# Optimization experiments

Measured on AMD Instinct MI355X. Metric: run time of the kernel, lower is better.

Reference implementation:

```python
import jax, jax.numpy as jnp
import numpy as np

EPS = 0.1
N_ITERS = 20


def setup_inputs() -> dict:
    key = jax.random.key(0)
    B, N = 8, 2048
    D = jax.random.normal(key, (B, N, N), dtype=jnp.float32)
    mask = jnp.ones((B, N), dtype=bool)
    return {"D": D, "mask": mask}


def reference(D, mask):
    # pad_2d[b,i,j] = True if row i or col j is padding
    pad_col = ~mask[:, None, :]          # [B,1,N]
    pad_row = ~mask[:, :, None]          # [B,N,1]
    pad_2d = pad_col | pad_row           # [B,N,N]
    log_K = jnp.where(pad_2d, -jnp.inf, -D / EPS)

    def body(lk, _):
        lk = lk - jax.nn.logsumexp(lk, axis=2, keepdims=True)  # row normalize
        lk = lk - jax.nn.logsumexp(lk, axis=1, keepdims=True)  # col normalize
        return lk, None

    log_K, _ = jax.lax.scan(body, log_K, None, length=N_ITERS)
    P = jnp.exp(log_K)
    n_real = jnp.maximum(mask.sum(axis=1).astype(D.dtype), 1.0)  # clamp(min=1)
    per_sample = (P * D).sum(axis=(1, 2)) / n_real
    return per_sample.mean()
```

## Files before the change

kernel.cpp:

```cpp
#include <hip/hip_runtime.h>


#ifndef __has_builtin
#define __has_builtin(x) 0
#endif

__device__ __forceinline__ float ex2(float x) {
#if __has_builtin(__builtin_amdgcn_exp2f)
  return __builtin_amdgcn_exp2f(x);
#else
  return exp2f(x);
#endif
}
__device__ __forceinline__ float lg2(float x) {
#if __has_builtin(__builtin_amdgcn_logf)
  return __builtin_amdgcn_logf(x);
#else
  return __log2f(x);
#endif
}

constexpr int   Bc    = 8;
constexpr int   Nc    = 2048;
constexpr int   NBLK  = 256;
constexpr int   NTHR  = 512;
constexpr int   WPB   = 8;
constexpr int   RPW   = 8;
constexpr int   RPB   = 64;
constexpr int   SL    = 32;
constexpr int   NIT   = 20;
constexpr int   FB    = 64;
constexpr float K2    = -14.426950408889634f;
constexpr float SCALE = -4.2306346e-06f;

__device__ __forceinline__ float f16lo(unsigned u) {
  return (float)__builtin_bit_cast(_Float16, (unsigned short)(u & 0xffffu));
}
__device__ __forceinline__ float f16hi(unsigned u) {
  return (float)__builtin_bit_cast(_Float16, (unsigned short)(u >> 16));
}
__device__ __forceinline__ unsigned packh(float x, float y) {
  unsigned short hx = __builtin_bit_cast(unsigned short, (_Float16)x);
  unsigned short hy = __builtin_bit_cast(unsigned short, (_Float16)y);
  return (unsigned)hx | ((unsigned)hy << 16);
}

typedef float fx4 __attribute__((ext_vector_type(4)));

__device__ __forceinline__ void st_sc(float* p, float4 v) {
  fx4 vv;
  vv.x = v.x; vv.y = v.y; vv.z = v.z; vv.w = v.w;
  asm volatile("global_store_dwordx4 %0, %1, off sc0 sc1"
               :
               : "v"(p), "v"(vv)
               : "memory");
}
__device__ __forceinline__ void st_sc1(float* p, float v) {
  asm volatile("global_store_dword %0, %1, off sc0 sc1"
               :
               : "v"(p), "v"(v)
               : "memory");
}

__device__ __forceinline__ void arrive(unsigned* f, unsigned epv) {
  asm volatile("s_waitcnt vmcnt(0)" ::: "memory");
  __syncthreads();
  if (threadIdx.x == 0)
    __hip_atomic_store(f, epv, __ATOMIC_RELAXED, __HIP_MEMORY_SCOPE_AGENT);
}
__device__ __forceinline__ void waitfor(const unsigned* fb_, unsigned epv) {
  const int t = threadIdx.x;
  if (t < 64) {
    bool ok = (t >= SL);
    for (;;) {
      if (t < SL)
        ok = __hip_atomic_load(&fb_[t], __ATOMIC_RELAXED,
                               __HIP_MEMORY_SCOPE_AGENT) >= epv;
      if (__ballot(ok) == ~0ull) break;
      __builtin_amdgcn_s_sleep(2);
    }
  }
  __syncthreads();
}

__global__ void k_init(unsigned* flags, float* out) {
  __hip_atomic_store(&flags[threadIdx.x], 0u, __ATOMIC_RELAXED,
                     __HIP_MEMORY_SCOPE_AGENT);
  if (threadIdx.x == 0)
    __hip_atomic_store(out, 0.f, __ATOMIC_RELAXED, __HIP_MEMORY_SCOPE_AGENT);
}

__global__ __launch_bounds__(NTHR, 2) void sink(const float* __restrict__ D,
                                                _Float16* __restrict__ A,
                                                float* __restrict__ Sp,
                                                float* __restrict__ Tp,
                                                float* __restrict__ cg,
                                                unsigned* __restrict__ f1,
                                                unsigned* __restrict__ f2,
                                                float* __restrict__ out) {
  __shared__ float colpart[WPB * Nc];
  __shared__ float cl[Nc];
  __shared__ float rl[RPB];

  const int t    = threadIdx.x;
  const int lane = t & 63;
  const int w    = t >> 6;
  const int blk  = blockIdx.x;
  const int b    = blk >> 5;
  const int s    = blk & 31;
  const long long row0 = (long long)b * Nc + (long long)s * RPB;
  unsigned* f1b = f1 + b * FB;
  unsigned* f2b = f2 + b * FB;

  if (t == 0) __builtin_amdgcn_fence(__ATOMIC_ACQUIRE, "agent");
  __syncthreads();

  for (int r = 0; r < RPW; ++r) {
    long long grow = row0 + (w * RPW + r);
    const float* dp = D + grow * Nc + lane * 8;
    _Float16*    ap = A + grow * Nc + lane * 8;
    #pragma unroll
    for (int c = 0; c < 4; ++c) {
      float4 x0 = *(const float4*)(dp + c * 512);
      float4 x1 = *(const float4*)(dp + c * 512 + 4);
      uint4 h;
      h.x = packh(K2 * x0.x, K2 * x0.y);
      h.y = packh(K2 * x0.z, K2 * x0.w);
      h.z = packh(K2 * x1.x, K2 * x1.y);
      h.w = packh(K2 * x1.z, K2 * x1.w);
      *(uint4*)(ap + c * 512) = h;
    }
  }
  for (int j = t; j < Nc; j += NTHR) cl[j] = 0.f;
  if (t < RPB) rl[t] = 0.f;
  __syncthreads();

  const _Float16* abase = A + (row0 + (long long)w * RPW) * Nc + lane * 8;

  #pragma unroll 1
  for (int it = 0; it < NIT; ++it) {
    const unsigned epv = (unsigned)(it + 1);
    const bool lastIt = (it == NIT - 1);
    float* SpIt = Sp + (size_t)it * (NBLK * Nc);
    float* cgIt = cg + (size_t)it * (Bc * Nc);

    float cs[32];
    #pragma unroll
    for (int c = 0; c < 4; ++c) {
      float4 q0 = *(const float4*)&cl[c * 512 + lane * 8];
      float4 q1 = *(const float4*)&cl[c * 512 + lane * 8 + 4];
      cs[c * 8 + 0] = q0.x; cs[c * 8 + 1] = q0.y; cs[c * 8 + 2] = q0.z; cs[c * 8 + 3] = q0.w;
      cs[c * 8 + 4] = q1.x; cs[c * 8 + 5] = q1.y; cs[c * 8 + 6] = q1.z; cs[c * 8 + 7] = q1.w;
    }
    float colacc[32], colaccT[32];
    #pragma unroll
    for (int k = 0; k < 32; ++k) { colacc[k] = 0.f; colaccT[k] = 0.f; }

    auto process = [&](const uint4 (&bf)[4], int lrow) {
      float shift = rl[lrow];
      const unsigned uu[16] = {bf[0].x, bf[0].y, bf[0].z, bf[0].w,
                               bf[1].x, bf[1].y, bf[1].z, bf[1].w,
                               bf[2].x, bf[2].y, bf[2].z, bf[2].w,
                               bf[3].x, bf[3].y, bf[3].z, bf[3].w};
      float e[32];
      float rs = 0.f;
      #pragma unroll
      for (int q = 0; q < 16; ++q) {
        float e0 = ex2(f16lo(uu[q]) - cs[2 * q] - shift);
        float e1 = ex2(f16hi(uu[q]) - cs[2 * q + 1] - shift);
        e[2 * q] = e0; e[2 * q + 1] = e1;
        rs += e0 + e1;
      }
      #pragma unroll
      for (int off = 1; off < 64; off <<= 1) rs += __shfl_xor(rs, off, 64);
      float inv = 1.0f / rs;
      #pragma unroll
      for (int k = 0; k < 32; ++k) colacc[k] += e[k] * inv;
      if (lastIt) {
        #pragma unroll
        for (int q = 0; q < 16; ++q) {
          colaccT[2 * q]     += e[2 * q] * inv * f16lo(uu[q]);
          colaccT[2 * q + 1] += e[2 * q + 1] * inv * f16hi(uu[q]);
        }
      }
      if (lane == 0) rl[lrow] = shift + lg2(rs);
    };

    uint4 cA[4], cB[4];
    #pragma unroll
    for (int c = 0; c < 4; ++c) cA[c] = *(const uint4*)(abase + c * 512);
    #pragma unroll
    for (int c = 0; c < 4; ++c) cB[c] = *(const uint4*)(abase + Nc + c * 512);
    #pragma unroll 1
    for (int rp = 0; rp < RPW / 2; ++rp) {
      uint4 nA[4], nB[4];
      #pragma unroll
      for (int c = 0; c < 4; ++c) { nA[c] = cA[c]; nB[c] = cB[c]; }
      if (rp < RPW / 2 - 1) {
        const _Float16* ap = abase + (size_t)(2 * rp + 2) * Nc;
        #pragma unroll
        for (int c = 0; c < 4; ++c) nA[c] = *(const uint4*)(ap + c * 512);
        #pragma unroll
        for (int c = 0; c < 4; ++c) nB[c] = *(const uint4*)(ap + Nc + c * 512);
      }
      process(cA, w * RPW + 2 * rp);
      process(cB, w * RPW + 2 * rp + 1);
      #pragma unroll
      for (int c = 0; c < 4; ++c) { cA[c] = nA[c]; cB[c] = nB[c]; }
    }

    #pragma unroll
    for (int c = 0; c < 4; ++c) {
      *(float4*)&colpart[w * Nc + c * 512 + lane * 8] =
          make_float4(colacc[c * 8 + 0], colacc[c * 8 + 1], colacc[c * 8 + 2], colacc[c * 8 + 3]);
      *(float4*)&colpart[w * Nc + c * 512 + lane * 8 + 4] =
          make_float4(colacc[c * 8 + 4], colacc[c * 8 + 5], colacc[c * 8 + 6], colacc[c * 8 + 7]);
    }
    __syncthreads();
    {
      int j0 = t * 4;
      float4 v = *(const float4*)&colpart[j0];
      #pragma unroll
      for (int g = 1; g < WPB; ++g) {
        float4 u = *(const float4*)&colpart[g * Nc + j0];
        v.x += u.x; v.y += u.y; v.z += u.z; v.w += u.w;
      }
      st_sc(SpIt + (size_t)blk * Nc + j0, v);
    }
    if (lastIt) {
      __syncthreads();
      #pragma unroll
      for (int c = 0; c < 4; ++c) {
        *(float4*)&colpart[w * Nc + c * 512 + lane * 8] =
            make_float4(colaccT[c * 8 + 0], colaccT[c * 8 + 1], colaccT[c * 8 + 2], colaccT[c * 8 + 3]);
        *(float4*)&colpart[w * Nc + c * 512 + lane * 8 + 4] =
            make_float4(colaccT[c * 8 + 4], colaccT[c * 8 + 5], colaccT[c * 8 + 6], colaccT[c * 8 + 7]);
      }
      __syncthreads();
      int j0 = t * 4;
      float4 v = *(const float4*)&colpart[j0];
      #pragma unroll
      for (int g = 1; g < WPB; ++g) {
        float4 u = *(const float4*)&colpart[g * Nc + j0];
        v.x += u.x; v.y += u.y; v.z += u.z; v.w += u.w;
      }
      st_sc(Tp + (size_t)blk * Nc + j0, v);
    }

    arrive(&f1b[s], epv);
    waitfor(f1b, epv);

    if (!lastIt) {
      {
        int colL = t & 63, slg = t >> 6;
        const float* bb = SpIt + (size_t)(b * SL) * Nc + s * 64 + colL;
        float v = 0.f;
        #pragma unroll
        for (int k = 0; k < 4; ++k) v += bb[(slg + 8 * k) * Nc];
        colpart[slg * 64 + colL] = v;
      }
      __syncthreads();
      if (t < 64) {
        float S = 0.f;
        #pragma unroll
        for (int g = 0; g < 8; ++g) S += colpart[g * 64 + t];
        st_sc1(cgIt + (size_t)b * Nc + s * 64 + t, cl[s * 64 + t] + lg2(S));
      }
      arrive(&f2b[s], epv);
      waitfor(f2b, epv);
      {
        int j0 = t * 4;
        float4 v = *(const float4*)(cgIt + (size_t)b * Nc + j0);
        *(float4*)&cl[j0] = v;
      }
      __syncthreads();
    } else {
      {
        int colL = t & 63, slg = t >> 6;
        const float* bbS = SpIt + (size_t)(b * SL) * Nc + s * 64 + colL;
        const float* bbT = Tp + (size_t)(b * SL) * Nc + s * 64 + colL;
        float vS = 0.f, vT = 0.f;
        #pragma unroll
        for (int k = 0; k < 4; ++k) {
          vS += bbS[(slg + 8 * k) * Nc];
          vT += bbT[(slg + 8 * k) * Nc];
        }
        colpart[slg * 64 + colL] = vS;
        colpart[512 + slg * 64 + colL] = vT;
      }
      __syncthreads();
      float q = 0.f;
      if (t < 64) {
        float S = 0.f, T = 0.f;
        #pragma unroll
        for (int g = 0; g < 8; ++g) {
          S += colpart[g * 64 + t];
          T += colpart[512 + g * 64 + t];
        }
        q = T / S;
        #pragma unroll
        for (int off = 32; off > 0; off >>= 1) q += __shfl_down(q, off, 64);
        if (t == 0) atomicAdd(out, q * SCALE);
      }
    }
  }
}

extern "C" void kernel_launch(void* const* d_in, const int* in_sizes, int n_in,
                              void* d_out, int out_size, void* d_ws, size_t ws_size,
                              hipStream_t stream) {
  const float* D = (const float*)d_in[0];
  char* p = (char*)d_ws;
  _Float16* A  = (_Float16*)p;  p += (size_t)Bc * Nc * Nc * 2;
  float*    Sp = (float*)p;     p += (size_t)NIT * NBLK * Nc * 4;
  float*    Tp = (float*)p;     p += (size_t)NBLK * Nc * 4;
  float*    cg = (float*)p;     p += (size_t)NIT * Bc * Nc * 4;
  unsigned* flags = (unsigned*)p;
  unsigned* f1 = flags;
  unsigned* f2 = flags + Bc * FB;

  k_init<<<1, 1024, 0, stream>>>(flags, (float*)d_out);
  sink<<<NBLK, NTHR, 0, stream>>>(D, A, Sp, Tp, cg, f1, f2, (float*)d_out);
}
```

Before: 580.1 us.

## Double block count to 512 with 32 rows each and reuse single-iteration scratch

Halves rows per block (32 instead of 64) and launches 512 persistent blocks, 64 slices per batch, so each CU holds two resident blocks and all CUs get work. Cross-block column reductions now span 64 slices with 32 columns each. Scratch buffers Sp and cg are no longer indexed per iteration; they are reused, with atomic relaxed loads so stale cached values are not read. This cuts the workspace footprint, but reuse relies on the flag barriers ordering writes of the next iteration after reads of the previous one, and there are twice as many blocks to synchronise.

```diff
diff --git a/kernel.cpp b/kernel.cpp
--- a/kernel.cpp
+++ b/kernel.cpp
@@ -22,12 +22,12 @@
 
 constexpr int   Bc    = 8;
 constexpr int   Nc    = 2048;
-constexpr int   NBLK  = 256;
+constexpr int   NBLK  = 512;
 constexpr int   NTHR  = 512;
 constexpr int   WPB   = 8;
-constexpr int   RPW   = 8;
-constexpr int   RPB   = 64;
-constexpr int   SL    = 32;
+constexpr int   RPW   = 4;
+constexpr int   RPB   = 32;
+constexpr int   SL    = 64;
 constexpr int   NIT   = 20;
 constexpr int   FB    = 64;
 constexpr float K2    = -14.426950408889634f;
@@ -60,6 +60,9 @@
                :
                : "v"(p), "v"(v)
                : "memory");
+}
+__device__ __forceinline__ float ald(const float* p) {
+  return __hip_atomic_load(p, __ATOMIC_RELAXED, __HIP_MEMORY_SCOPE_AGENT);
 }
 
 __device__ __forceinline__ void arrive(unsigned* f, unsigned epv) {
@@ -106,8 +109,8 @@
   const int lane = t & 63;
   const int w    = t >> 6;
   const int blk  = blockIdx.x;
-  const int b    = blk >> 5;
-  const int s    = blk & 31;
+  const int b    = blk >> 6;
+  const int s    = blk & 63;
   const long long row0 = (long long)b * Nc + (long long)s * RPB;
   unsigned* f1b = f1 + b * FB;
   unsigned* f2b = f2 + b * FB;
@@ -141,8 +144,6 @@
   for (int it = 0; it < NIT; ++it) {
     const unsigned epv = (unsigned)(it + 1);
     const bool lastIt = (it == NIT - 1);
-    float* SpIt = Sp + (size_t)it * (NBLK * Nc);
-    float* cgIt = cg + (size_t)it * (Bc * Nc);
 
     float cs[32];
     #pragma unroll
@@ -225,7 +226,7 @@
         float4 u = *(const float4*)&colpart[g * Nc + j0];
         v.x += u.x; v.y += u.y; v.z += u.z; v.w += u.w;
       }
-      st_sc(SpIt + (size_t)blk * Nc + j0, v);
+      st_sc(Sp + (size_t)blk * Nc + j0, v);
     }
     if (lastIt) {
       __syncthreads();
@@ -252,52 +253,53 @@
 
     if (!lastIt) {
       {
-        int colL = t & 63, slg = t >> 6;
-        const float* bb = SpIt + (size_t)(b * SL) * Nc + s * 64 + colL;
+        int colL = t & 31, slg = t >> 5;
+        const float* bb = Sp + (size_t)(b * SL) * Nc + s * 32 + colL;
         float v = 0.f;
         #pragma unroll
-        for (int k = 0; k < 4; ++k) v += bb[(slg + 8 * k) * Nc];
-        colpart[slg * 64 + colL] = v;
-      }
-      __syncthreads();
-      if (t < 64) {
+        for (int k = 0; k < 4; ++k) v += ald(&bb[(size_t)(slg + 16 * k) * Nc]);
+        colpart[slg * 32 + colL] = v;
+      }
+      __syncthreads();
+      if (t < 32) {
         float S = 0.f;
         #pragma unroll
-        for (int g = 0; g < 8; ++g) S += colpart[g * 64 + t];
-        st_sc1(cgIt + (size_t)b * Nc + s * 64 + t, cl[s * 64 + t] + lg2(S));
+        for (int g = 0; g < 16; ++g) S += colpart[g * 32 + t];
+        st_sc1(cg + (size_t)b * Nc + s * 32 + t, cl[s * 32 + t] + lg2(S));
       }
       arrive(&f2b[s], epv);
       waitfor(f2b, epv);
       {
-        int j0 = t * 4;
-        float4 v = *(const float4*)(cgIt + (size_t)b * Nc + j0);
-        *(float4*)&cl[j0] = v;
+        const float* cgb = cg + (size_t)b * Nc;
+        for (int j = t; j < Nc; j += NTHR) cl[j] = ald(cgb + j);
       }
       __syncthreads();
     } else {
       {
-        int colL = t & 63, slg = t >> 6;
-        const float* bbS = SpIt + (size_t)(b * SL) * Nc + s * 64 + colL;
-        const float* bbT = Tp + (size_t)(b * SL) * Nc + s * 64 + colL;
+        int colL = t & 31, slg = t >> 5;
+        const float* bbS = Sp + (size_t)(b * SL) * Nc + s * 32 + colL;
+        const float* bbT = Tp + (size_t)(b * SL) * Nc + s * 32 + colL;
         float vS = 0.f, vT = 0.f;
         #pragma unroll
         for (int k = 0; k < 4; ++k) {
-          vS += bbS[(slg + 8 * k) * Nc];
-          vT += bbT[(slg + 8 * k) * Nc];
+          vS += ald(&bbS[(size_t)(slg + 16 * k) * Nc]);
+          vT += ald(&bbT[(size_t)(slg + 16 * k) * Nc]);
         }
-        colpart[slg * 64 + colL] = vS;
-        colpart[512 + slg * 64 + colL] = vT;
-      }
-      __syncthreads();
-      float q = 0.f;
+        colpart[slg * 32 + colL] = vS;
+        colpart[512 + slg * 32 + colL] = vT;
+      }
+      __syncthreads();
       if (t < 64) {
-        float S = 0.f, T = 0.f;
-        #pragma unroll
-        for (int g = 0; g < 8; ++g) {
-          S += colpart[g * 64 + t];
-          T += colpart[512 + g * 64 + t];
+        float q = 0.f;
+        if (t < 32) {
+          float S = 0.f, T = 0.f;
+          #pragma unroll
+          for (int g = 0; g < 16; ++g) {
+            S += colpart[g * 32 + t];
+            T += colpart[512 + g * 32 + t];
+          }
+          q = T / S;
         }
-        q = T / S;
         #pragma unroll
         for (int off = 32; off > 0; off >>= 1) q += __shfl_down(q, off, 64);
         if (t == 0) atomicAdd(out, q * SCALE);
@@ -312,9 +314,9 @@
   const float* D = (const float*)d_in[0];
   char* p = (char*)d_ws;
   _Float16* A  = (_Float16*)p;  p += (size_t)Bc * Nc * Nc * 2;
-  float*    Sp = (float*)p;     p += (size_t)NIT * NBLK * Nc * 4;
+  float*    Sp = (float*)p;     p += (size_t)NBLK * Nc * 4;
   float*    Tp = (float*)p;     p += (size_t)NBLK * Nc * 4;
-  float*    cg = (float*)p;     p += (size_t)NIT * Bc * Nc * 4;
+  float*    cg = (float*)p;     p += (size_t)Bc * Nc * 4;
   unsigned* flags = (unsigned*)p;
   unsigned* f1 = flags;
   unsigned* f2 = flags + Bc * FB;
```

New measurement: 960.0 us. 1.65x slower.

## Stage first rows in LDS and replace global barriers with per-producer flag polling

Applied to the files above, without the earlier changes.

Keeps the first two rows per wave resident in shared memory, so each iteration starts processing without a global load. It also replaces the full-batch barrier waits on f1/f2 with per-source flag polling, so each wave consumes partial sums from a producer block as soon as that block has arrived. This aims to cut barrier stall time and load latency at the start of each iteration. It adds 64KB of LDS, which may reduce occupancy at two blocks per CU. It also relies on relaxed atomic loads plus a compiler barrier for ordering, which is a memory-ordering risk.

```diff
diff --git a/kernel.cpp b/kernel.cpp
--- a/kernel.cpp
+++ b/kernel.cpp
@@ -101,6 +101,7 @@
   __shared__ float colpart[WPB * Nc];
   __shared__ float cl[Nc];
   __shared__ float rl[RPB];
+  __shared__ _Float16 astage[16 * Nc];
 
   const int t    = threadIdx.x;
   const int lane = t & 63;
@@ -129,6 +130,8 @@
       h.z = packh(K2 * x1.x, K2 * x1.y);
       h.w = packh(K2 * x1.z, K2 * x1.w);
       *(uint4*)(ap + c * 512) = h;
+      if (r < 2)
+        *(uint4*)&astage[(w * 2 + r) * Nc + c * 512 + lane * 8] = h;
     }
   }
   for (int j = t; j < Nc; j += NTHR) cl[j] = 0.f;
@@ -186,16 +189,25 @@
       if (lane == 0) rl[lrow] = shift + lg2(rs);
     };
 
-    uint4 cA[4], cB[4];
-    #pragma unroll
-    for (int c = 0; c < 4; ++c) cA[c] = *(const uint4*)(abase + c * 512);
-    #pragma unroll
-    for (int c = 0; c < 4; ++c) cB[c] = *(const uint4*)(abase + Nc + c * 512);
+    uint4 pA[4], pB[4], nA[4], nB[4];
+    #pragma unroll
+    for (int c = 0; c < 4; ++c) {
+      pA[c] = *(const uint4*)&astage[(w * 2 + 0) * Nc + c * 512 + lane * 8];
+      pB[c] = *(const uint4*)&astage[(w * 2 + 1) * Nc + c * 512 + lane * 8];
+    }
+    {
+      const _Float16* ap = abase + (size_t)2 * Nc;
+      #pragma unroll
+      for (int c = 0; c < 4; ++c) nA[c] = *(const uint4*)(ap + c * 512);
+      #pragma unroll
+      for (int c = 0; c < 4; ++c) nB[c] = *(const uint4*)(ap + Nc + c * 512);
+    }
+    process(pA, w * RPW + 0);
+    process(pB, w * RPW + 1);
     #pragma unroll 1
-    for (int rp = 0; rp < RPW / 2; ++rp) {
-      uint4 nA[4], nB[4];
-      #pragma unroll
-      for (int c = 0; c < 4; ++c) { nA[c] = cA[c]; nB[c] = cB[c]; }
+    for (int rp = 1; rp < RPW / 2; ++rp) {
+      #pragma unroll
+      for (int c = 0; c < 4; ++c) { pA[c] = nA[c]; pB[c] = nB[c]; }
       if (rp < RPW / 2 - 1) {
         const _Float16* ap = abase + (size_t)(2 * rp + 2) * Nc;
         #pragma unroll
@@ -203,10 +215,8 @@
         #pragma unroll
         for (int c = 0; c < 4; ++c) nB[c] = *(const uint4*)(ap + Nc + c * 512);
       }
-      process(cA, w * RPW + 2 * rp);
-      process(cB, w * RPW + 2 * rp + 1);
-      #pragma unroll
-      for (int c = 0; c < 4; ++c) { cA[c] = nA[c]; cB[c] = nB[c]; }
+      process(pA, w * RPW + 2 * rp);
+      process(pB, w * RPW + 2 * rp + 1);
     }
 
     #pragma unroll
@@ -248,16 +258,28 @@
     }
 
     arrive(&f1b[s], epv);
-    waitfor(f1b, epv);
 
     if (!lastIt) {
       {
-        int colL = t & 63, slg = t >> 6;
-        const float* bb = SpIt + (size_t)(b * SL) * Nc + s * 64 + colL;
+        const float* bb = SpIt + (size_t)(b * SL) * Nc + s * 64 + lane;
         float v = 0.f;
-        #pragma unroll
-        for (int k = 0; k < 4; ++k) v += bb[(slg + 8 * k) * Nc];
-        colpart[slg * 64 + colL] = v;
+        unsigned done = 0;
+        while (done != 0xFu) {
+          #pragma unroll
+          for (int k = 0; k < 4; ++k) {
+            if (!(done & (1u << k))) {
+              unsigned fv = __hip_atomic_load(&f1b[w + 8 * k], __ATOMIC_RELAXED,
+                                              __HIP_MEMORY_SCOPE_AGENT);
+              if (fv >= epv) {
+                asm volatile("" ::: "memory");
+                v += bb[(size_t)(w + 8 * k) * Nc];
+                done |= (1u << k);
+              }
+            }
+          }
+          if (done != 0xFu) __builtin_amdgcn_s_sleep(1);
+        }
+        colpart[w * 64 + lane] = v;
       }
       __syncthreads();
       if (t < 64) {
@@ -267,14 +289,29 @@
         st_sc1(cgIt + (size_t)b * Nc + s * 64 + t, cl[s * 64 + t] + lg2(S));
       }
       arrive(&f2b[s], epv);
-      waitfor(f2b, epv);
       {
-        int j0 = t * 4;
-        float4 v = *(const float4*)(cgIt + (size_t)b * Nc + j0);
-        *(float4*)&cl[j0] = v;
+        const float* cgb = cgIt + (size_t)b * Nc;
+        unsigned done = 0;
+        while (done != 0xFu) {
+          #pragma unroll
+          for (int k = 0; k < 4; ++k) {
+            if (!(done & (1u << k))) {
+              int c = w + 8 * k;
+              unsigned fv = __hip_atomic_load(&f2b[c], __ATOMIC_RELAXED,
+                                              __HIP_MEMORY_SCOPE_AGENT);
+              if (fv >= epv) {
+                asm volatile("" ::: "memory");
+                cl[c * 64 + lane] = cgb[c * 64 + lane];
+                done |= (1u << k);
+              }
+            }
+          }
+          if (done != 0xFu) __builtin_amdgcn_s_sleep(1);
+        }
       }
       __syncthreads();
     } else {
+      waitfor(f1b, epv);
       {
         int colL = t & 63, slg = t >> 6;
         const float* bbS = SpIt + (size_t)(b * SL) * Nc + s * 64 + colL;
```

After: 633.7 us. 1.09x slower.
